# Performance work log

Measured on AMD Instinct MI355X. Metric: run time of the kernel, lower is better.

The kernel has to match this reference:

```python
import jax, jax.numpy as jnp
import numpy as np

C = 64
G = 4
K = 3
GC = C // G
OS = 1.0  # offset_scale
OM_DIM = int(np.ceil(G * K * K * 3 / 8) * 8)  # 112, padded; only first G*27 used


def setup_inputs() -> dict:
    key = jax.random.key(0)
    ks = jax.random.split(key, 8)
    B, H, W = 2, 384, 384
    s = 0.02
    return {
        "inp": jax.random.normal(ks[0], (B, C, H, W), jnp.float32),
        "Wv": jax.random.normal(ks[1], (C, C), jnp.float32) * s,
        "bv": jnp.zeros((C,), jnp.float32),
        "Wdw": jax.random.normal(ks[2], (C, 1, K, K), jnp.float32) * s,
        "bdw": jnp.zeros((C,), jnp.float32),
        "Wom": jax.random.normal(ks[3], (C, OM_DIM), jnp.float32) * s,
        "bom": jnp.zeros((OM_DIM,), jnp.float32),
        "Wo": jax.random.normal(ks[4], (C, C), jnp.float32) * s,
    }


def _bilinear(v, px, py, H, W, b_idx, g_idx):
    # v: (B,H,W,G,GC); px,py: (B,H,W,G) pixel coords; zero padding outside.
    x0 = jnp.floor(px)
    y0 = jnp.floor(py)
    wx1 = px - x0
    wy1 = py - y0
    x0i = x0.astype(jnp.int32)
    y0i = y0.astype(jnp.int32)
    out = jnp.zeros(px.shape + (v.shape[-1],), v.dtype)
    for dy, wy in ((0, 1.0 - wy1), (1, wy1)):
        for dx, wx in ((0, 1.0 - wx1), (1, wx1)):
            xi = x0i + dx
            yi = y0i + dy
            valid = ((xi >= 0) & (xi < W) & (yi >= 0) & (yi < H)).astype(v.dtype)
            xc = jnp.clip(xi, 0, W - 1)
            yc = jnp.clip(yi, 0, H - 1)
            g = v[b_idx, yc, xc, g_idx]  # (B,H,W,G,GC)
            out = out + g * (wy * wx * valid)[..., None]
    return out


def reference(inp, Wv, bv, Wdw, bdw, Wom, bom, Wo):
    B, _, H, W = inp.shape
    x = inp.transpose(0, 2, 3, 1)  # (B,H,W,C)
    # value projection, split into groups
    value = (x @ Wv + bv).reshape(B, H, W, G, GC)
    # depthwise conv on input feeds the offset/mask predictor
    dw = jax.lax.conv_general_dilated(
        inp, Wdw, window_strides=(1, 1), padding=[(1, 1), (1, 1)],
        feature_group_count=C) + bdw[None, :, None, None]
    om = dw.transpose(0, 2, 3, 1) @ Wom + bom  # (B,H,W,OM_DIM)
    om = om[..., : G * K * K * 3].reshape(B, H, W, G, K * K * 3)
    off = om[..., : K * K * 2].reshape(B, H, W, G, K * K, 2)  # (dx,dy) per point
    mask = om[..., K * K * 2:]  # (B,H,W,G,K*K), no softmax in DCNv4

    base_x = jnp.arange(W, dtype=value.dtype)[None, None, :, None]
    base_y = jnp.arange(H, dtype=value.dtype)[None, :, None, None]
    b_idx = jnp.arange(B)[:, None, None, None]
    g_idx = jnp.arange(G)[None, None, None, :]

    out = jnp.zeros((B, H, W, G, GC), value.dtype)
    k = 0
    for ky in range(K):
        for kx in range(K):
            dx = off[..., k, 0]
            dy = off[..., k, 1]
            px = base_x + ((kx - K // 2) + dx) * OS
            py = base_y + ((ky - K // 2) + dy) * OS
            samp = _bilinear(value, px, py, H, W, b_idx, g_idx)
            out = out + samp * mask[..., k][..., None]
            k += 1

    out = out.reshape(B, H, W, C) @ Wo  # output_proj, no bias (output_bias=False)
    return out.transpose(0, 3, 1, 2)  # back to (B,C,H,W)
```

## Files before the change

### kernel.cpp

```cpp
#include <hip/hip_runtime.h>
#include <hip/hip_fp16.h>
#include <math.h>

namespace {
constexpr int kH = 384, kW = 384, kBn = 2;
constexpr int kHW = kH * kW;
constexpr int kOMD = 112;
constexpr int kNB = kBn * (kHW / 64);
constexpr int kNB8 = kNB / 8;
}

typedef _Float16 h2 __attribute__((ext_vector_type(2)));
typedef _Float16 half8 __attribute__((ext_vector_type(8)));
typedef float f32x4 __attribute__((ext_vector_type(4)));

__device__ unsigned g_Wom2[32 * kOMD];
__device__ unsigned g_Wo2[32 * 64];
__device__ __align__(16) _Float16 g_WvFh[4 * 2 * 64 * 8];
__device__ __align__(16) _Float16 g_WvFl[4 * 2 * 64 * 8];

__device__ __forceinline__ int swz(int t) {
    return (t & 7) * kNB8 + (t >> 3);
}

__device__ __forceinline__ unsigned pack2h(float a, float b) {
    unsigned short lo = __builtin_bit_cast(unsigned short, __float2half_rn(a));
    unsigned short hi = __builtin_bit_cast(unsigned short, __float2half_rn(b));
    return (unsigned)lo | ((unsigned)hi << 16);
}

__device__ __forceinline__ unsigned packhh(_Float16 a, _Float16 b) {
    const unsigned short ua = __builtin_bit_cast(unsigned short, a);
    const unsigned short ub = __builtin_bit_cast(unsigned short, b);
    return (unsigned)ua | ((unsigned)ub << 16);
}

#if __has_builtin(__builtin_amdgcn_fdot2)
__device__ __forceinline__ float dot2(unsigned a, unsigned b, float c) {
    return __builtin_amdgcn_fdot2(__builtin_bit_cast(h2, a),
                                  __builtin_bit_cast(h2, b), c, false);
}
#else
__device__ __forceinline__ float dot2(unsigned a, unsigned b, float c) {
    h2 ha = __builtin_bit_cast(h2, a), hb = __builtin_bit_cast(h2, b);
    c = fmaf((float)ha.x, (float)hb.x, c);
    c = fmaf((float)ha.y, (float)hb.y, c);
    return c;
}
#endif

__device__ __forceinline__ void acc8h(__half2* pa, const unsigned short* src,
                                      float wgt) {
    const uint4 u0 = ((const uint4*)src)[0];
    const uint4 u1 = ((const uint4*)src)[1];
    const __half2 w2 = __half2half2(__float2half_rn(wgt));
    pa[0] = __hfma2(w2, __builtin_bit_cast(__half2, u0.x), pa[0]);
    pa[1] = __hfma2(w2, __builtin_bit_cast(__half2, u0.y), pa[1]);
    pa[2] = __hfma2(w2, __builtin_bit_cast(__half2, u0.z), pa[2]);
    pa[3] = __hfma2(w2, __builtin_bit_cast(__half2, u0.w), pa[3]);
    pa[4] = __hfma2(w2, __builtin_bit_cast(__half2, u1.x), pa[4]);
    pa[5] = __hfma2(w2, __builtin_bit_cast(__half2, u1.y), pa[5]);
    pa[6] = __hfma2(w2, __builtin_bit_cast(__half2, u1.z), pa[6]);
    pa[7] = __hfma2(w2, __builtin_bit_cast(__half2, u1.w), pa[7]);
}

__device__ __forceinline__ half8 ld_frag_g(const _Float16* ptr) {
    return __builtin_bit_cast(half8, *(const uint4*)ptr);
}

__global__ __launch_bounds__(256) void k_prep(
        const float* __restrict__ Wv, const float* __restrict__ Wom,
        const float* __restrict__ Wo) {
    const int tid = threadIdx.x;
    for (int i = tid; i < 4 * 2 * 64 * 8; i += 256) {
        const int jj = i & 7, l = (i >> 3) & 63, kh = (i >> 9) & 1, mt = i >> 10;
        const int co = mt * 16 + (l & 15);
        const int ch = kh * 32 + ((l >> 4) & 3) * 8 + jj;
        const float w = Wv[ch * 64 + co];
        const _Float16 hi = (_Float16)w;
        g_WvFh[i] = hi;
        g_WvFl[i] = (_Float16)((w - (float)hi) * 2048.f);
    }
    for (int i = tid; i < 32 * kOMD; i += 256) {
        const int ci2 = i / kOMD, j = i % kOMD;
        g_Wom2[i] = pack2h(Wom[(2 * ci2) * kOMD + j],
                           Wom[(2 * ci2 + 1) * kOMD + j]);
    }
    for (int i = tid; i < 32 * 64; i += 256) {
        const int ci2 = i >> 6, j = i & 63;
        g_Wo2[i] = pack2h(Wo[(2 * ci2) * 64 + j],
                          Wo[(2 * ci2 + 1) * 64 + j]);
    }
}

__global__ __launch_bounds__(256) void k_value(
        const float* __restrict__ inp, const float* __restrict__ bv,
        unsigned short* __restrict__ value) {
    __shared__ unsigned xh[8][64][4];
    __shared__ unsigned xl[8][64][4];
    const int tid = threadIdx.x;
    const int bid = swz(blockIdx.x);
    const int b = bid / (kHW / 64);
    const int pix0 = (bid % (kHW / 64)) * 64;
    const float* ib = inp + (size_t)b * 64 * kHW + pix0;

    #pragma unroll
    for (int it = 0; it < 2; ++it) {
        const int i = tid + it * 256;
        const int c8 = i >> 6, px = i & 63;
        const float* src = ib + (size_t)(c8 * 8) * kHW + px;
        unsigned uh[4], ul[4];
        #pragma unroll
        for (int e = 0; e < 4; ++e) {
            const float x0 = src[(size_t)(2 * e) * kHW];
            const float x1 = src[(size_t)(2 * e + 1) * kHW];
            const _Float16 h0 = (_Float16)x0, h1 = (_Float16)x1;
            const _Float16 l0 = (_Float16)((x0 - (float)h0) * 2048.f);
            const _Float16 l1 = (_Float16)((x1 - (float)h1) * 2048.f);
            uh[e] = packhh(h0, h1);
            ul[e] = packhh(l0, l1);
        }
        *(uint4*)&xh[c8][px][0] = make_uint4(uh[0], uh[1], uh[2], uh[3]);
        *(uint4*)&xl[c8][px][0] = make_uint4(ul[0], ul[1], ul[2], ul[3]);
    }
    __syncthreads();

    const int l = tid & 63;
    const int wv = __builtin_amdgcn_readfirstlane(tid >> 6);
    const int lr = l & 15, q = l >> 4;
    const int px = wv * 16 + lr;

    half8 bhf[2], blf[2];
    #pragma unroll
    for (int kh = 0; kh < 2; ++kh) {
        bhf[kh] = __builtin_bit_cast(half8, *(const uint4*)&xh[kh * 4 + q][px][0]);
        blf[kh] = __builtin_bit_cast(half8, *(const uint4*)&xl[kh * 4 + q][px][0]);
    }
    #pragma unroll
    for (int mt = 0; mt < 4; ++mt) {
        const half8 ah0 = ld_frag_g(g_WvFh + ((mt * 2 + 0) * 64 + l) * 8);
        const half8 ah1 = ld_frag_g(g_WvFh + ((mt * 2 + 1) * 64 + l) * 8);
        const half8 al0 = ld_frag_g(g_WvFl + ((mt * 2 + 0) * 64 + l) * 8);
        const half8 al1 = ld_frag_g(g_WvFl + ((mt * 2 + 1) * 64 + l) * 8);
        f32x4 acc = {0.f, 0.f, 0.f, 0.f};
        f32x4 acc2 = {0.f, 0.f, 0.f, 0.f};
        acc  = __builtin_amdgcn_mfma_f32_16x16x32_f16(ah0, bhf[0], acc, 0, 0, 0);
        acc  = __builtin_amdgcn_mfma_f32_16x16x32_f16(ah1, bhf[1], acc, 0, 0, 0);
        acc2 = __builtin_amdgcn_mfma_f32_16x16x32_f16(ah0, blf[0], acc2, 0, 0, 0);
        acc2 = __builtin_amdgcn_mfma_f32_16x16x32_f16(ah1, blf[1], acc2, 0, 0, 0);
        acc2 = __builtin_amdgcn_mfma_f32_16x16x32_f16(al0, bhf[0], acc2, 0, 0, 0);
        acc2 = __builtin_amdgcn_mfma_f32_16x16x32_f16(al1, bhf[1], acc2, 0, 0, 0);
        const float4 b4 = *(const float4*)(bv + mt * 16 + q * 4);
        const float v0 = acc[0] + acc2[0] * (1.f / 2048.f) + b4.x;
        const float v1 = acc[1] + acc2[1] * (1.f / 2048.f) + b4.y;
        const float v2 = acc[2] + acc2[2] * (1.f / 2048.f) + b4.z;
        const float v3 = acc[3] + acc2[3] * (1.f / 2048.f) + b4.w;
        uint2 st;
        st.x = pack2h(v0, v1);
        st.y = pack2h(v2, v3);
        *(uint2*)(value + ((size_t)(b * 4 + mt) * kHW + pix0 + px) * 16 + q * 4) = st;
    }
}

__global__ __launch_bounds__(256) void k_main(
        const float* __restrict__ inp, const float* __restrict__ Wdw,
        const float* __restrict__ bdw, const float* __restrict__ bom,
        const unsigned short* __restrict__ value, float* __restrict__ out) {
    __shared__ unsigned lds2[32][64];

    const int tid = threadIdx.x;
    const int bid = swz(blockIdx.x);
    const int b = bid / (kH * (kW / 64));
    const int rem = bid % (kH * (kW / 64));
    const int h = rem / (kW / 64);
    const int w0 = (rem % (kW / 64)) * 64;

    const int p = tid & 63;
    const int gs = __builtin_amdgcn_readfirstlane(tid >> 6);

    {
        const int w = w0 + p;
        #pragma unroll 2
        for (int q = 0; q < 8; ++q) {
            float sv[2];
            #pragma unroll
            for (int e = 0; e < 2; ++e) {
                const int c = gs * 16 + 2 * q + e;
                const float* ib = inp + (size_t)(b * 64 + c) * kHW;
                float s = bdw[c];
                #pragma unroll
                for (int r = 0; r < 3; ++r) {
                    const int y = h - 1 + r;
                    if (y >= 0 && y < kH) {
                        const float* rowp = ib + (size_t)y * kW;
                        #pragma unroll
                        for (int kx = 0; kx < 3; ++kx) {
                            const int x = w - 1 + kx;
                            const float v = (x >= 0 && x < kW) ? rowp[x] : 0.f;
                            s = fmaf(v, Wdw[c * 9 + r * 3 + kx], s);
                        }
                    }
                }
                sv[e] = s;
            }
            lds2[gs * 8 + q][p] = pack2h(sv[0], sv[1]);
        }
    }
    __syncthreads();

    float om[27];
    {
        const float* bg = bom + gs * 27;
        #pragma unroll
        for (int j = 0; j < 27; ++j) om[j] = bg[j];
        #pragma unroll 4
        for (int ci2 = 0; ci2 < 32; ++ci2) {
            const unsigned a2 = lds2[ci2][p];
            const unsigned* wr = g_Wom2 + ci2 * kOMD + gs * 27;
            #pragma unroll
            for (int j = 0; j < 27; ++j) om[j] = dot2(a2, wr[j], om[j]);
        }
    }
    __syncthreads();

    {
        __half2 pa[8];
        #pragma unroll
        for (int j = 0; j < 8; ++j) pa[j] = __builtin_bit_cast(__half2, 0u);
        const float fw = (float)(w0 + p);
        const float fh = (float)h;
        const unsigned short* vbase = value + (size_t)(b * 4 + gs) * kHW * 16;
        #pragma unroll
        for (int k = 0; k < 9; ++k) {
            const int ky = k / 3, kx = k % 3;
            const float dx = om[2 * k];
            const float dy = om[2 * k + 1];
            const float m = om[18 + k];
            const float px = fw + (float)(kx - 1) + dx;
            const float py = fh + (float)(ky - 1) + dy;
            const float x0f = floorf(px), y0f = floorf(py);
            const int x0 = (int)x0f, y0 = (int)y0f;
            const float wx1 = px - x0f, wy1 = py - y0f;
            const float wx0 = 1.f - wx1, wy0 = 1.f - wy1;
            const bool interior = (x0 >= 0) & (y0 >= 0) &
                                  (x0 < kW - 1) & (y0 < kH - 1);
            if (__all(interior)) {
                const unsigned short* b00 = vbase + ((size_t)y0 * kW + x0) * 16;
                const float wy0m = wy0 * m, wy1m = wy1 * m;
                acc8h(pa, b00,                wx0 * wy0m);
                acc8h(pa, b00 + 16,           wx1 * wy0m);
                acc8h(pa, b00 + kW * 16,      wx0 * wy1m);
                acc8h(pa, b00 + kW * 16 + 16, wx1 * wy1m);
            } else {
                #pragma unroll
                for (int cor = 0; cor < 4; ++cor) {
                    const int dy2 = cor >> 1, dx2 = cor & 1;
                    const int xi = x0 + dx2, yi = y0 + dy2;
                    float wgt = (dy2 ? wy1 : wy0) * (dx2 ? wx1 : wx0) * m;
                    if (xi < 0 || xi >= kW || yi < 0 || yi >= kH) wgt = 0.f;
                    const int xc = min(max(xi, 0), kW - 1);
                    const int yc = min(max(yi, 0), kH - 1);
                    acc8h(pa, vbase + ((size_t)yc * kW + xc) * 16, wgt);
                }
            }
        }
        #pragma unroll
        for (int j = 0; j < 8; ++j)
            lds2[gs * 8 + j][p] = __builtin_bit_cast(unsigned, pa[j]);
    }
    __syncthreads();

    {
        float acc[16];
        #pragma unroll
        for (int j = 0; j < 16; ++j) acc[j] = 0.f;
        #pragma unroll 4
        for (int ci2 = 0; ci2 < 32; ++ci2) {
            const unsigned a2 = lds2[ci2][p];
            const unsigned* wr = g_Wo2 + ci2 * 64 + gs * 16;
            #pragma unroll
            for (int j = 0; j < 16; ++j) acc[j] = dot2(a2, wr[j], acc[j]);
        }
        float* ob = out + (size_t)(b * 64 + gs * 16) * kHW + (size_t)h * kW + w0 + p;
        #pragma unroll
        for (int j = 0; j < 16; ++j) ob[(size_t)j * kHW] = acc[j];
    }
}

extern "C" void kernel_launch(void* const* d_in, const int* in_sizes, int n_in,
                              void* d_out, int out_size, void* d_ws, size_t ws_size,
                              hipStream_t stream) {
    const float* inp = (const float*)d_in[0];
    const float* Wv  = (const float*)d_in[1];
    const float* bv  = (const float*)d_in[2];
    const float* Wdw = (const float*)d_in[3];
    const float* bdw = (const float*)d_in[4];
    const float* Wom = (const float*)d_in[5];
    const float* bom = (const float*)d_in[6];
    const float* Wo  = (const float*)d_in[7];
    float* outp = (float*)d_out;
    unsigned short* value = (unsigned short*)d_ws;

    k_prep<<<1, 256, 0, stream>>>(Wv, Wom, Wo);
    k_value<<<kNB, 256, 0, stream>>>(inp, bv, value);
    k_main<<<kNB, 256, 0, stream>>>(inp, Wdw, bdw, bom, value, outp);
}
```

Baseline: 306.7 us.

## Load value-projection inputs directly to registers, vectorize interior depthwise conv, parallelize prep

k_value drops its LDS staging and __syncthreads, and each lane now loads its 16 input channels straight from global memory into MFMA fragments, splitting each value into hi and lo fp16 parts in registers. In k_main, interior column tiles take a new depthwise-conv path where each thread computes two adjacent pixels from float2 loads plus left and right neighbours. That path halves per-pixel loads and writes packed results to LDS in a different thread-to-channel layout. k_prep is launched with 64 blocks instead of one to shorten the serial weight-packing prologue; the direct loads give up LDS coalescing, and the edge tiles keep the old conv path.

```diff
diff --git a/kernel.cpp b/kernel.cpp
--- a/kernel.cpp
+++ b/kernel.cpp
@@ -27,12 +27,6 @@
     unsigned short lo = __builtin_bit_cast(unsigned short, __float2half_rn(a));
     unsigned short hi = __builtin_bit_cast(unsigned short, __float2half_rn(b));
     return (unsigned)lo | ((unsigned)hi << 16);
-}
-
-__device__ __forceinline__ unsigned packhh(_Float16 a, _Float16 b) {
-    const unsigned short ua = __builtin_bit_cast(unsigned short, a);
-    const unsigned short ub = __builtin_bit_cast(unsigned short, b);
-    return (unsigned)ua | ((unsigned)ub << 16);
 }
 
 #if __has_builtin(__builtin_amdgcn_fdot2)
@@ -71,8 +65,9 @@
 __global__ __launch_bounds__(256) void k_prep(
         const float* __restrict__ Wv, const float* __restrict__ Wom,
         const float* __restrict__ Wo) {
-    const int tid = threadIdx.x;
-    for (int i = tid; i < 4 * 2 * 64 * 8; i += 256) {
+    const int gt = blockIdx.x * 256 + threadIdx.x;
+    const int gstep = 64 * 256;
+    for (int i = gt; i < 4 * 2 * 64 * 8; i += gstep) {
         const int jj = i & 7, l = (i >> 3) & 63, kh = (i >> 9) & 1, mt = i >> 10;
         const int co = mt * 16 + (l & 15);
         const int ch = kh * 32 + ((l >> 4) & 3) * 8 + jj;
@@ -81,12 +76,12 @@
         g_WvFh[i] = hi;
         g_WvFl[i] = (_Float16)((w - (float)hi) * 2048.f);
     }
-    for (int i = tid; i < 32 * kOMD; i += 256) {
+    for (int i = gt; i < 32 * kOMD; i += gstep) {
         const int ci2 = i / kOMD, j = i % kOMD;
         g_Wom2[i] = pack2h(Wom[(2 * ci2) * kOMD + j],
                            Wom[(2 * ci2 + 1) * kOMD + j]);
     }
-    for (int i = tid; i < 32 * 64; i += 256) {
+    for (int i = gt; i < 32 * 64; i += gstep) {
         const int ci2 = i >> 6, j = i & 63;
         g_Wo2[i] = pack2h(Wo[(2 * ci2) * 64 + j],
                           Wo[(2 * ci2 + 1) * 64 + j]);
@@ -96,46 +91,34 @@
 __global__ __launch_bounds__(256) void k_value(
         const float* __restrict__ inp, const float* __restrict__ bv,
         unsigned short* __restrict__ value) {
-    __shared__ unsigned xh[8][64][4];
-    __shared__ unsigned xl[8][64][4];
     const int tid = threadIdx.x;
     const int bid = swz(blockIdx.x);
     const int b = bid / (kHW / 64);
     const int pix0 = (bid % (kHW / 64)) * 64;
-    const float* ib = inp + (size_t)b * 64 * kHW + pix0;
-
-    #pragma unroll
-    for (int it = 0; it < 2; ++it) {
-        const int i = tid + it * 256;
-        const int c8 = i >> 6, px = i & 63;
-        const float* src = ib + (size_t)(c8 * 8) * kHW + px;
-        unsigned uh[4], ul[4];
-        #pragma unroll
-        for (int e = 0; e < 4; ++e) {
-            const float x0 = src[(size_t)(2 * e) * kHW];
-            const float x1 = src[(size_t)(2 * e + 1) * kHW];
-            const _Float16 h0 = (_Float16)x0, h1 = (_Float16)x1;
-            const _Float16 l0 = (_Float16)((x0 - (float)h0) * 2048.f);
-            const _Float16 l1 = (_Float16)((x1 - (float)h1) * 2048.f);
-            uh[e] = packhh(h0, h1);
-            ul[e] = packhh(l0, l1);
-        }
-        *(uint4*)&xh[c8][px][0] = make_uint4(uh[0], uh[1], uh[2], uh[3]);
-        *(uint4*)&xl[c8][px][0] = make_uint4(ul[0], ul[1], ul[2], ul[3]);
-    }
-    __syncthreads();
-
     const int l = tid & 63;
-    const int wv = __builtin_amdgcn_readfirstlane(tid >> 6);
+    const int wv = tid >> 6;
     const int lr = l & 15, q = l >> 4;
-    const int px = wv * 16 + lr;
-
+    const int gpx = pix0 + wv * 16 + lr;
+
+    const float* xb = inp + (size_t)b * 64 * kHW + (size_t)(q * 8) * kHW + gpx;
     half8 bhf[2], blf[2];
     #pragma unroll
     for (int kh = 0; kh < 2; ++kh) {
-        bhf[kh] = __builtin_bit_cast(half8, *(const uint4*)&xh[kh * 4 + q][px][0]);
-        blf[kh] = __builtin_bit_cast(half8, *(const uint4*)&xl[kh * 4 + q][px][0]);
-    }
+        float xv[8];
+        #pragma unroll
+        for (int jj = 0; jj < 8; ++jj)
+            xv[jj] = xb[(size_t)(kh * 32 + jj) * kHW];
+        half8 hh, ll;
+        #pragma unroll
+        for (int jj = 0; jj < 8; ++jj) {
+            const _Float16 hval = (_Float16)xv[jj];
+            hh[jj] = hval;
+            ll[jj] = (_Float16)((xv[jj] - (float)hval) * 2048.f);
+        }
+        bhf[kh] = hh;
+        blf[kh] = ll;
+    }
+
     #pragma unroll
     for (int mt = 0; mt < 4; ++mt) {
         const half8 ah0 = ld_frag_g(g_WvFh + ((mt * 2 + 0) * 64 + l) * 8);
@@ -158,7 +141,7 @@
         uint2 st;
         st.x = pack2h(v0, v1);
         st.y = pack2h(v2, v3);
-        *(uint2*)(value + ((size_t)(b * 4 + mt) * kHW + pix0 + px) * 16 + q * 4) = st;
+        *(uint2*)(value + ((size_t)(b * 4 + mt) * kHW + gpx) * 16 + q * 4) = st;
     }
 }
 
@@ -178,7 +161,50 @@
     const int p = tid & 63;
     const int gs = __builtin_amdgcn_readfirstlane(tid >> 6);
 
-    {
+    if (w0 != 0 && w0 != kW - 64) {
+        const int i2 = p & 31;
+        const int ch8 = p >> 5;
+        const int xg = w0 + 2 * i2;
+        float s0[8], s1[8];
+        #pragma unroll 4
+        for (int cc = 0; cc < 8; ++cc) {
+            const int cA = gs * 16 + cc;
+            const int cB = cA + 8;
+            const float bsv = ch8 ? bdw[cB] : bdw[cA];
+            float a0 = bsv, a1 = bsv;
+            const float* ibA = inp + (size_t)(b * 64 + cA) * kHW;
+            const float* wkA = Wdw + cA * 9;
+            const float* wkB = Wdw + cB * 9;
+            #pragma unroll
+            for (int r = 0; r < 3; ++r) {
+                const int y = h - 1 + r;
+                if (y >= 0 && y < kH) {
+                    const float* rowp = ibA + (size_t)(ch8 * 8) * kHW
+                                            + (size_t)y * kW;
+                    const float2 fc = *(const float2*)(rowp + xg);
+                    const float xl = rowp[xg - 1];
+                    const float xr = rowp[xg + 2];
+                    const float k0 = ch8 ? wkB[r * 3 + 0] : wkA[r * 3 + 0];
+                    const float k1 = ch8 ? wkB[r * 3 + 1] : wkA[r * 3 + 1];
+                    const float k2 = ch8 ? wkB[r * 3 + 2] : wkA[r * 3 + 2];
+                    a0 = fmaf(xl,   k0, a0);
+                    a0 = fmaf(fc.x, k1, a0);
+                    a0 = fmaf(fc.y, k2, a0);
+                    a1 = fmaf(fc.x, k0, a1);
+                    a1 = fmaf(fc.y, k1, a1);
+                    a1 = fmaf(xr,   k2, a1);
+                }
+            }
+            s0[cc] = a0;
+            s1[cc] = a1;
+        }
+        #pragma unroll
+        for (int e = 0; e < 4; ++e) {
+            const int row = gs * 8 + ch8 * 4 + e;
+            lds2[row][2 * i2]     = pack2h(s0[2 * e], s0[2 * e + 1]);
+            lds2[row][2 * i2 + 1] = pack2h(s1[2 * e], s1[2 * e + 1]);
+        }
+    } else {
         const int w = w0 + p;
         #pragma unroll 2
         for (int q = 0; q < 8; ++q) {
@@ -301,7 +327,7 @@
     float* outp = (float*)d_out;
     unsigned short* value = (unsigned short*)d_ws;
 
-    k_prep<<<1, 256, 0, stream>>>(Wv, Wom, Wo);
+    k_prep<<<64, 256, 0, stream>>>(Wv, Wom, Wo);
     k_value<<<kNB, 256, 0, stream>>>(inp, bv, value);
     k_main<<<kNB, 256, 0, stream>>>(inp, Wdw, bdw, bom, value, outp);
 }
```

Result: faster. 299.1 us (-2.5%).
